# Optimization experiments

Hardware: AMD Instinct MI355X
Metric: run time of the kernel (lower is better)

The kernel has to match this reference:

```python
import jax, jax.numpy as jnp
import numpy as np

B, S, N, H, C = 64, 512, 24, 768, 6

CONST_LAST = jnp.array([0.1, 0.1, 0.1, 0.3, 0.8, 0.01], dtype=jnp.float32)
CONST_MID = jnp.array([0.1, 0.1, 0.1, 0.8, 0.3, 0.01], dtype=jnp.float32)


def setup_inputs() -> dict:
    key = jax.random.key(0)
    k1, k2, k3, k4 = jax.random.split(key, 4)
    last_hidden_state = jax.random.normal(k1, (B, S, H), dtype=jnp.float32)
    # strictly increasing boundaries in [0, S-1]: sort randint in [0, S-N) then add arange(N)
    base = jnp.sort(jax.random.randint(k2, (B, N), 0, S - N), axis=1)
    sentence_token = base + jnp.arange(N, dtype=base.dtype)[None, :]
    W = jax.random.normal(k3, (C, H), dtype=jnp.float32) * 0.02
    b = jax.random.normal(k4, (C,), dtype=jnp.float32) * 0.02
    return {"last_hidden_state": last_hidden_state, "sentence_token": sentence_token,
            "W": W, "b": b}


def reference(last_hidden_state, sentence_token, W, b):
    # last_hidden_state: [B,S,H]; sentence_token: [B,N] strictly increasing boundaries.
    # Segment j covers tokens [prev+1, t_j] inclusive (prev = -1 for j==0).
    ends = sentence_token                                            # [B,N]
    prev = jnp.concatenate([-jnp.ones_like(ends[:, :1]), ends[:, :-1]], axis=1)
    # prefix sums with leading zero: csp[:, t+1] = sum of tokens 0..t
    cs = jnp.cumsum(last_hidden_state, axis=1)                       # [B,S,H]
    csp = jnp.concatenate([jnp.zeros_like(cs[:, :1]), cs], axis=1)   # [B,S+1,H]
    seg_sum = (jnp.take_along_axis(csp, (ends + 1)[:, :, None], axis=1)
               - jnp.take_along_axis(csp, (prev + 1)[:, :, None], axis=1))  # [B,N,H]
    lens = (ends - prev).astype(last_hidden_state.dtype)[:, :, None]  # >= 1 by construction
    seg_mean = seg_sum / lens                                         # [B,N,H]
    probs = jax.nn.sigmoid(jnp.einsum('bnh,ch->bnc', seg_mean, W) + b)  # [B,N,C]
    # override: boundary > 500 -> constant probability vector (different if last sentence)
    is_last = (jnp.arange(ends.shape[1]) == ends.shape[1] - 1)[None, :, None]  # [1,N,1]
    const = jnp.where(is_last, CONST_LAST[None, None, :], CONST_MID[None, None, :])
    over = (ends > 500)[:, :, None]
    return jnp.where(over, const, probs)
```

## Files before the change

### kernel.cpp

```cpp
#include <hip/hip_runtime.h>
#include <math.h>

#define B_ 64
#define S_ 512
#define N_ 24
#define H_ 768
#define C_ 6
#define CHUNKS 16
#define TOK_PER_BLOCK (S_ / CHUNKS)
#define TOK_PER_WAVE (TOK_PER_BLOCK/4)

__device__ __forceinline__ void do_token(const float4 x[3], const float4 w[3][C_],
                                         int seg, int lane, float* acc) {
  float a[C_];
#pragma unroll
  for (int c = 0; c < C_; ++c) a[c] = 0.f;
#pragma unroll
  for (int k = 0; k < 3; ++k)
#pragma unroll
    for (int c = 0; c < C_; ++c)
      a[c] += x[k].x * w[k][c].x + x[k].y * w[k][c].y +
              x[k].z * w[k][c].z + x[k].w * w[k][c].w;
#pragma unroll
  for (int c = 0; c < C_; ++c)
    atomicAdd(&acc[(seg * C_ + c) * 64 + lane], a[c]);
}

__global__ __launch_bounds__(256, 4) void seg_proj_kernel(
    const float* __restrict__ lhs, const int* __restrict__ st,
    const float* __restrict__ W, float* __restrict__ outbuf, int use_atomic) {
  __shared__ float acc[N_ * C_ * 64];
  const int tid = threadIdx.x;
  const int lane = tid & 63;
  const int wave = tid >> 6;
  const int b = blockIdx.x / CHUNKS;
  const int chunk = blockIdx.x % CHUNKS;

  for (int i = tid; i < N_ * C_ * 64; i += 256) acc[i] = 0.f;

  int stb_l = st[b * N_ + (lane < N_ ? lane : N_ - 1)];
  int last = __shfl(stb_l, N_ - 1, 64);

  const float4* W4 = (const float4*)W;
  float4 w[3][C_];
#pragma unroll
  for (int k = 0; k < 3; ++k)
#pragma unroll
    for (int c = 0; c < C_; ++c)
      w[k][c] = W4[c * (H_ / 4) + k * 64 + lane];

  __syncthreads();

  const int s_base = chunk * TOK_PER_BLOCK + wave * TOK_PER_WAVE;
#pragma unroll
  for (int g = 0; g < TOK_PER_WAVE / 2; ++g) {
    const int s0 = s_base + g * 2;
    const bool a0 = (s0 <= last);
    const bool a1 = (s0 + 1 <= last);
    const float4* x4 = (const float4*)(lhs + ((size_t)b * S_ + s0) * H_);
    float4 x0[3], x1[3];
    if (a0) {
      x0[0] = x4[lane]; x0[1] = x4[64 + lane]; x0[2] = x4[128 + lane];
    }
    if (a1) {
      x1[0] = x4[192 + lane]; x1[1] = x4[256 + lane]; x1[2] = x4[320 + lane];
    }
    if (a0) {
      unsigned long long m = __ballot(lane < N_ && stb_l < s0);
      do_token(x0, w, (int)__popcll(m), lane, acc);
    }
    if (a1) {
      unsigned long long m = __ballot(lane < N_ && stb_l < s0 + 1);
      do_token(x1, w, (int)__popcll(m), lane, acc);
    }
  }

  __syncthreads();
  if (tid < N_ * C_) {
    float v = 0.f;
    const int base = tid * 64;
#pragma unroll 8
    for (int i = 0; i < 64; ++i) v += acc[base + ((i + tid) & 63)];
    if (use_atomic)
      atomicAdd(&outbuf[b * N_ * C_ + tid], v);
    else
      outbuf[(size_t)blockIdx.x * (N_ * C_) + tid] = v;
  }
}

__global__ __launch_bounds__(256) void finalize_kernel(
    const float* __restrict__ buf, const int* __restrict__ st,
    const float* __restrict__ bias, float* __restrict__ out, int use_atomic) {
  int idx = blockIdx.x * blockDim.x + threadIdx.x;
  if (idx >= B_ * N_ * C_) return;
  int c = idx % C_;
  int j = (idx / C_) % N_;
  int b = idx / (N_ * C_);
  float ssum;
  if (use_atomic) {
    ssum = buf[idx];
  } else {
    ssum = 0.f;
#pragma unroll
    for (int k = 0; k < CHUNKS; ++k)
      ssum += buf[(size_t)(b * CHUNKS + k) * (N_ * C_) + j * C_ + c];
  }
  int end = st[b * N_ + j];
  int prev = (j == 0) ? -1 : st[b * N_ + j - 1];
  float len = (float)(end - prev);
  float logit = ssum / len + bias[c];
  float p = 1.0f / (1.0f + expf(-logit));
  if (end > 500) {
    float cl = (c < 3) ? 0.1f : (c == 3 ? 0.3f : (c == 4 ? 0.8f : 0.01f));
    float cm = (c < 3) ? 0.1f : (c == 3 ? 0.8f : (c == 4 ? 0.3f : 0.01f));
    p = (j == N_ - 1) ? cl : cm;
  }
  out[idx] = p;
}

extern "C" void kernel_launch(void* const* d_in, const int* in_sizes, int n_in,
                              void* d_out, int out_size, void* d_ws, size_t ws_size,
                              hipStream_t stream) {
  const float* lhs  = (const float*)d_in[0];
  const int*   st   = (const int*)d_in[1];
  const float* W    = (const float*)d_in[2];
  const float* bias = (const float*)d_in[3];

  const size_t need = (size_t)B_ * CHUNKS * N_ * C_ * sizeof(float);
  const int use_atomic = (ws_size < need) ? 1 : 0;
  if (use_atomic)
    hipMemsetAsync(d_ws, 0, (size_t)B_ * N_ * C_ * sizeof(float), stream);

  seg_proj_kernel<<<B_ * CHUNKS, 256, 0, stream>>>(lhs, st, W, (float*)d_ws, use_atomic);
  finalize_kernel<<<(B_ * N_ * C_ + 255) / 256, 256, 0, stream>>>(
      (float*)d_ws, st, bias, (float*)d_out, use_atomic);
}
```

Before: 186.3 us.

## Preload all wave tokens up front and accumulate per segment in registers

Each wave now issues loads for all its 8 tokens at once instead of pairs, which puts more memory requests in flight. Partial dot products are accumulated in registers and flushed to shared memory only when the segment index changes, so there are fewer LDS atomics. The tail skip for tokens past the last boundary is removed: tokens after the last boundary fall into segment N and are dropped, but their data is still loaded. Launch bounds drop to 2 blocks per CU to make room for the extra registers, and an asm barrier keeps the weights resident in VGPRs.

```diff
diff --git a/kernel.cpp b/kernel.cpp
--- a/kernel.cpp
+++ b/kernel.cpp
@@ -8,25 +8,9 @@
 #define C_ 6
 #define CHUNKS 16
 #define TOK_PER_BLOCK (S_ / CHUNKS)
-#define TOK_PER_WAVE (TOK_PER_BLOCK/4)
+#define TOK_PER_WAVE (TOK_PER_BLOCK / 4)
 
-__device__ __forceinline__ void do_token(const float4 x[3], const float4 w[3][C_],
-                                         int seg, int lane, float* acc) {
-  float a[C_];
-#pragma unroll
-  for (int c = 0; c < C_; ++c) a[c] = 0.f;
-#pragma unroll
-  for (int k = 0; k < 3; ++k)
-#pragma unroll
-    for (int c = 0; c < C_; ++c)
-      a[c] += x[k].x * w[k][c].x + x[k].y * w[k][c].y +
-              x[k].z * w[k][c].z + x[k].w * w[k][c].w;
-#pragma unroll
-  for (int c = 0; c < C_; ++c)
-    atomicAdd(&acc[(seg * C_ + c) * 64 + lane], a[c]);
-}
-
-__global__ __launch_bounds__(256, 4) void seg_proj_kernel(
+__global__ __launch_bounds__(256, 2) void seg_proj_kernel(
     const float* __restrict__ lhs, const int* __restrict__ st,
     const float* __restrict__ W, float* __restrict__ outbuf, int use_atomic) {
   __shared__ float acc[N_ * C_ * 64];
@@ -36,10 +20,12 @@
   const int b = blockIdx.x / CHUNKS;
   const int chunk = blockIdx.x % CHUNKS;
 
-  for (int i = tid; i < N_ * C_ * 64; i += 256) acc[i] = 0.f;
+  float4* accv = (float4*)acc;
+#pragma unroll
+  for (int i = 0; i < 9; ++i)
+    accv[i * 256 + tid] = make_float4(0.f, 0.f, 0.f, 0.f);
 
-  int stb_l = st[b * N_ + (lane < N_ ? lane : N_ - 1)];
-  int last = __shfl(stb_l, N_ - 1, 64);
+  int stb_l = (lane < N_) ? st[b * N_ + lane] : 0x7fffffff;
 
   const float4* W4 = (const float4*)W;
   float4 w[3][C_];
@@ -48,31 +34,54 @@
 #pragma unroll
     for (int c = 0; c < C_; ++c)
       w[k][c] = W4[c * (H_ / 4) + k * 64 + lane];
+#pragma unroll
+  for (int k = 0; k < 3; ++k)
+    asm volatile("" : "+v"(w[k][0].x), "+v"(w[k][0].y), "+v"(w[k][0].z), "+v"(w[k][0].w),
+                       "+v"(w[k][1].x), "+v"(w[k][1].y), "+v"(w[k][1].z), "+v"(w[k][1].w),
+                       "+v"(w[k][2].x), "+v"(w[k][2].y), "+v"(w[k][2].z), "+v"(w[k][2].w),
+                       "+v"(w[k][3].x), "+v"(w[k][3].y), "+v"(w[k][3].z), "+v"(w[k][3].w),
+                       "+v"(w[k][4].x), "+v"(w[k][4].y), "+v"(w[k][4].z), "+v"(w[k][4].w),
+                       "+v"(w[k][5].x), "+v"(w[k][5].y), "+v"(w[k][5].z), "+v"(w[k][5].w));
 
   __syncthreads();
 
   const int s_base = chunk * TOK_PER_BLOCK + wave * TOK_PER_WAVE;
+  const float4* x4 = (const float4*)(lhs + ((size_t)b * S_ + s_base) * H_);
+  float4 x[TOK_PER_WAVE][3];
 #pragma unroll
-  for (int g = 0; g < TOK_PER_WAVE / 2; ++g) {
-    const int s0 = s_base + g * 2;
-    const bool a0 = (s0 <= last);
-    const bool a1 = (s0 + 1 <= last);
-    const float4* x4 = (const float4*)(lhs + ((size_t)b * S_ + s0) * H_);
-    float4 x0[3], x1[3];
-    if (a0) {
-      x0[0] = x4[lane]; x0[1] = x4[64 + lane]; x0[2] = x4[128 + lane];
+  for (int t = 0; t < TOK_PER_WAVE; ++t) {
+    x[t][0] = x4[t * 192 + lane];
+    x[t][1] = x4[t * 192 + 64 + lane];
+    x[t][2] = x4[t * 192 + 128 + lane];
+  }
+
+  float racc[C_] = {0.f, 0.f, 0.f, 0.f, 0.f, 0.f};
+  int cur_seg = N_;
+#pragma unroll
+  for (int t = 0; t < TOK_PER_WAVE; ++t) {
+    const int s = s_base + t;
+    const int seg = (int)__popcll(__ballot(stb_l < s));
+    if (seg != cur_seg) {
+      if (cur_seg < N_) {
+#pragma unroll
+        for (int c = 0; c < C_; ++c)
+          atomicAdd(&acc[(cur_seg * C_ + c) * 64 + lane], racc[c]);
+      }
+#pragma unroll
+      for (int c = 0; c < C_; ++c) racc[c] = 0.f;
+      cur_seg = seg;
     }
-    if (a1) {
-      x1[0] = x4[192 + lane]; x1[1] = x4[256 + lane]; x1[2] = x4[320 + lane];
-    }
-    if (a0) {
-      unsigned long long m = __ballot(lane < N_ && stb_l < s0);
-      do_token(x0, w, (int)__popcll(m), lane, acc);
-    }
-    if (a1) {
-      unsigned long long m = __ballot(lane < N_ && stb_l < s0 + 1);
-      do_token(x1, w, (int)__popcll(m), lane, acc);
-    }
+#pragma unroll
+    for (int k = 0; k < 3; ++k)
+#pragma unroll
+      for (int c = 0; c < C_; ++c)
+        racc[c] += x[t][k].x * w[k][c].x + x[t][k].y * w[k][c].y +
+                   x[t][k].z * w[k][c].z + x[t][k].w * w[k][c].w;
+  }
+  if (cur_seg < N_) {
+#pragma unroll
+    for (int c = 0; c < C_; ++c)
+      atomicAdd(&acc[(cur_seg * C_ + c) * 64 + lane], racc[c]);
   }
 
   __syncthreads();
```

New measurement: 153.9 us. 17.4% less time.
